# Optimization experiments

Measured on AMD Instinct MI355X. Metric: run time of the kernel, lower is better.

Reference implementation:

```python
import jax, jax.numpy as jnp
import numpy as np

HEADS = 8
EMBED = 128
HEAD_DIM = EMBED // HEADS


def setup_inputs() -> dict:
    key = jax.random.key(0)
    ks = jax.random.split(key, 6)
    s = 0.05
    return {
        "x": jax.random.normal(ks[0], (8, 128, 128, 128), dtype=jnp.float32),
        "Wq": jax.random.normal(ks[1], (HEAD_DIM, HEAD_DIM), dtype=jnp.float32) * s,
        "Wk": jax.random.normal(ks[2], (HEAD_DIM, HEAD_DIM), dtype=jnp.float32) * s,
        "Wv": jax.random.normal(ks[3], (HEAD_DIM, HEAD_DIM), dtype=jnp.float32) * s,
        "Wo": jax.random.normal(ks[4], (EMBED, EMBED), dtype=jnp.float32) * s,
        "bo": jnp.zeros((EMBED,), dtype=jnp.float32),
    }


def reference(x, Wq, Wk, Wv, Wo, bo):
    # is_width=False: attend along the H axis. x: [N, C, H, W]
    y = jnp.transpose(x, (0, 3, 2, 1))  # [N, W, H, C]
    N, D1, D2, C = y.shape
    y = y.reshape(N * D1, D2, HEADS, HEAD_DIM)  # [n, k, h, d]
    # nn.Linear applies y @ W.T
    q = jnp.einsum("nkhd,ed->nkhe", y, Wq)
    k = jnp.einsum("nkhd,ed->nkhe", y, Wk)
    v = jnp.einsum("nkhd,ed->nkhe", y, Wv)
    energy = jnp.einsum("nqhd,nkhd->nhqk", q, k)
    scale = jnp.asarray(EMBED, energy.dtype) ** 0.5  # note: original divides by sqrt(embed_size)
    attn = jax.nn.softmax(energy / scale, axis=-1)
    out = jnp.einsum("nhqk,nkhd->nqhd", attn, v).reshape(N, D1, D2, C)
    out = jnp.einsum("nqkc,ec->nqke", out, Wo) + bo
    return jnp.transpose(out, (0, 3, 2, 1))  # back to [N, C, H, W]
```

## Files before the change

kernel.cpp:

```cpp
#include <hip/hip_runtime.h>
#include <hip/hip_fp16.h>


typedef __attribute__((ext_vector_type(4))) float f32x4;
typedef __attribute__((ext_vector_type(4))) _Float16 f16x4;
typedef __attribute__((ext_vector_type(2))) __fp16 fp16x2r;
typedef __attribute__((ext_vector_type(8))) short bf16x8;

__device__ __forceinline__ unsigned int bf16_rne(float x) {
    unsigned int u = __float_as_uint(x);
    return (u + 0x7fffu + ((u >> 16) & 1u)) >> 16;
}
__device__ __forceinline__ unsigned int pack_half2(float a, float b) {
    __half2 h = __floats2half2_rn(a, b);
    return *reinterpret_cast<unsigned int*>(&h);
}

__global__ __launch_bounds__(1024, 4) void axattn_attn(
    const float* __restrict__ x,
    const float* __restrict__ Wq,
    const float* __restrict__ Wk,
    const float* __restrict__ Wv,
    const float* __restrict__ Wo,
    unsigned short* __restrict__ Wob,
    unsigned short* __restrict__ AO)
{
    int bb  = blockIdx.x;
    int xcd = bb & 7;
    int nh  = bb >> 3;
    int n0  = nh >> 3;
    int h   = nh & 7;
    int tid = threadIdx.x;
    int wvi = tid >> 6;
    int l   = tid & 63;
    int lr  = l & 15;
    int lg  = l >> 4;
    int w0  = xcd * 16;
    int w   = w0 + wvi;

    if (tid < 32) {
        int i = bb * 32 + tid;
        Wob[i] = (unsigned short)bf16_rne(Wo[i]);
    }

    __shared__ unsigned int xs[16 * 1280];

    {
        int q   = tid & 3;
        int row = (tid >> 2) & 127;
        int c2b = tid >> 9;
        const float* gp0 = x + ((size_t)(n0 * 128 + h * 16) * 128 + row) * 128 + w0 + q * 4;
        float4 va[4], vb[4];
        #pragma unroll
        for (int it = 0; it < 4; ++it) {
            const float* gp = gp0 + (size_t)(2 * (it * 2 + c2b)) * 16384;
            va[it] = *(const float4*)gp;
            vb[it] = *(const float4*)(gp + 16384);
        }
        #pragma unroll
        for (int it = 0; it < 4; ++it) {
            int c2 = it * 2 + c2b;
            unsigned int* dp = xs + (q * 4) * 1280 + row * 10 + c2;
            dp[0]    = pack_half2(va[it].x, vb[it].x);
            dp[1280] = pack_half2(va[it].y, vb[it].y);
            dp[2560] = pack_half2(va[it].z, vb[it].z);
            dp[3840] = pack_half2(va[it].w, vb[it].w);
        }
    }

    const float qsc = 0.088388347648318447f * 1.4426950408889634f;
    const f32x4 zf = {0.f, 0.f, 0.f, 0.f};

    float4 wqf = *(const float4*)(Wq + lr * 16 + lg * 4);
    float4 wkf = *(const float4*)(Wk + lr * 16 + lg * 4);
    float4 wvf = *(const float4*)(Wv + lr * 16 + lg * 4);
    f16x4 fq = {(_Float16)wqf.x, (_Float16)wqf.y, (_Float16)wqf.z, (_Float16)wqf.w};
    f16x4 fk = {(_Float16)wkf.x, (_Float16)wkf.y, (_Float16)wkf.z, (_Float16)wkf.w};
    f16x4 fv = {(_Float16)wvf.x, (_Float16)wvf.y, (_Float16)wvf.z, (_Float16)wvf.w};

    __syncthreads();

    const char* yb = (const char*)xs + wvi * 5120 + lr * 40 + lg * 8;
    f16x4 yf[8];
    #pragma unroll
    for (int rt = 0; rt < 8; ++rt)
        yf[rt] = *(const f16x4*)(yb + rt * 640);

    f16x4 qb[8], ka[8], vb[8];
    #pragma unroll
    for (int t = 0; t < 8; ++t) {
        f32x4 qt = __builtin_amdgcn_mfma_f32_16x16x16f16(fq, yf[t], zf, 0, 0, 0);
        f32x4 kt = __builtin_amdgcn_mfma_f32_16x16x16f16(fk, yf[t], zf, 0, 0, 0);
        f32x4 vt = __builtin_amdgcn_mfma_f32_16x16x16f16(yf[t], fv, zf, 0, 0, 0);
        qb[t] = (f16x4){(_Float16)(qt[0] * qsc), (_Float16)(qt[1] * qsc),
                        (_Float16)(qt[2] * qsc), (_Float16)(qt[3] * qsc)};
        ka[t] = (f16x4){(_Float16)kt[0], (_Float16)kt[1], (_Float16)kt[2], (_Float16)kt[3]};
        vb[t] = (f16x4){(_Float16)vt[0], (_Float16)vt[1], (_Float16)vt[2], (_Float16)vt[3]};
    }

    unsigned short* aob = AO + ((size_t)(n0 * 128 + w) * 128 + lg * 4) * 128 + h * 16 + lr;

    #pragma unroll
    for (int qt = 0; qt < 8; ++qt) {
        f32x4 s[8];
        #pragma unroll
        for (int kt = 0; kt < 8; ++kt)
            s[kt] = __builtin_amdgcn_mfma_f32_16x16x16f16(ka[kt], qb[qt], zf, 0, 0, 0);
        float sum = 0.f;
        f16x4 pa[8];
        #pragma unroll
        for (int kt = 0; kt < 8; ++kt) {
            float p0 = __builtin_amdgcn_exp2f(s[kt][0]);
            float p1 = __builtin_amdgcn_exp2f(s[kt][1]);
            float p2 = __builtin_amdgcn_exp2f(s[kt][2]);
            float p3 = __builtin_amdgcn_exp2f(s[kt][3]);
            sum += (p0 + p1) + (p2 + p3);
            union { fp16x2r h2[2]; f16x4 h4; } up;
            up.h2[0] = __builtin_amdgcn_cvt_pkrtz(p0, p1);
            up.h2[1] = __builtin_amdgcn_cvt_pkrtz(p2, p3);
            pa[kt] = up.h4;
        }
        sum += __shfl_xor(sum, 16);
        sum += __shfl_xor(sum, 32);
        f32x4 oA = zf, oB = zf;
        #pragma unroll
        for (int kt = 0; kt < 4; ++kt) {
            oA = __builtin_amdgcn_mfma_f32_16x16x16f16(pa[kt],     vb[kt],     oA, 0, 0, 0);
            oB = __builtin_amdgcn_mfma_f32_16x16x16f16(pa[kt + 4], vb[kt + 4], oB, 0, 0, 0);
        }
        f32x4 o = oA + oB;
        float rl = 1.f / sum;
        #pragma unroll
        for (int r = 0; r < 4; ++r) {
            float rs = __shfl(rl, lg * 4 + r);
            aob[((size_t)qt * 16 + r) * 128] = (unsigned short)bf16_rne(o[r] * rs);
        }
    }
}

__global__ __launch_bounds__(256) void axattn_proj(
    const unsigned short* __restrict__ AOb,
    const unsigned short* __restrict__ Wob,
    const float* __restrict__ bo,
    float* __restrict__ out)
{
    int bb  = blockIdx.x;
    int wh  = bb & 1;
    int s   = (bb >> 1) & 127;
    int n0  = bb >> 8;
    int tid = threadIdx.x;
    int wv  = tid >> 6;
    int l   = tid & 63;
    int lr  = l & 15;
    int lg  = l >> 4;
    int lk  = lg * 8;
    int eb  = wv * 32;

    __shared__ char as_[64 * 272];

    const unsigned short* wp_ = Wob + (size_t)(eb + lr) * 128 + lk;
    bf16x8 a0[4], a1[4];
    #pragma unroll
    for (int ct = 0; ct < 4; ++ct) {
        a0[ct] = *(const bf16x8*)(wp_ + ct * 32);
        a1[ct] = *(const bf16x8*)(wp_ + 16 * 128 + ct * 32);
    }

    {
        uint4 t4[4];
        #pragma unroll
        for (int it = 0; it < 4; ++it) {
            int flat = it * 256 + tid;
            int row  = flat >> 4;
            int seg  = flat & 15;
            t4[it] = *((const uint4*)(AOb
                + ((size_t)(n0 * 128 + wh * 64 + row) * 128 + s) * 128) + seg);
        }
        #pragma unroll
        for (int it = 0; it < 4; ++it) {
            int flat = it * 256 + tid;
            int row  = flat >> 4;
            int seg  = flat & 15;
            *(uint4*)(as_ + row * 272 + seg * 16) = t4[it];
        }
    }
    __syncthreads();

    f32x4 acc[2][4];
    #pragma unroll
    for (int mi = 0; mi < 2; ++mi)
        #pragma unroll
        for (int ni = 0; ni < 4; ++ni)
            acc[mi][ni] = (f32x4){0.f, 0.f, 0.f, 0.f};

    #pragma unroll
    for (int ct = 0; ct < 4; ++ct) {
        #pragma unroll
        for (int ni = 0; ni < 4; ++ni) {
            bf16x8 b = *(const bf16x8*)(as_ + (ni * 16 + lr) * 272 + (lk + ct * 32) * 2);
            acc[0][ni] = __builtin_amdgcn_mfma_f32_16x16x32_bf16(a0[ct], b, acc[0][ni], 0, 0, 0);
            acc[1][ni] = __builtin_amdgcn_mfma_f32_16x16x32_bf16(a1[ct], b, acc[1][ni], 0, 0, 0);
        }
    }

    int r4 = lg * 4;
    #pragma unroll
    for (int mi = 0; mi < 2; ++mi) {
        #pragma unroll
        for (int r = 0; r < 4; ++r) {
            int e = eb + mi * 16 + r4 + r;
            float bv = bo[e];
            float* orow = out + ((size_t)(n0 * 128 + e) * 128 + s) * 128 + wh * 64 + lr;
            #pragma unroll
            for (int ni = 0; ni < 4; ++ni)
                orow[ni * 16] = acc[mi][ni][r] + bv;
        }
    }
}

extern "C" void kernel_launch(void* const* d_in, const int* in_sizes, int n_in,
                              void* d_out, int out_size, void* d_ws, size_t ws_size,
                              hipStream_t stream) {
    const float* x  = (const float*)d_in[0];
    const float* Wq = (const float*)d_in[1];
    const float* Wk = (const float*)d_in[2];
    const float* Wv = (const float*)d_in[3];
    const float* Wo = (const float*)d_in[4];
    const float* bo = (const float*)d_in[5];
    float* out = (float*)d_out;

    unsigned short* AOb = (unsigned short*)d_ws;
    unsigned short* Wob = (unsigned short*)((char*)d_ws + (32u << 20));

    axattn_attn<<<512, 1024, 0, stream>>>(x, Wq, Wk, Wv, Wo, Wob, AOb);
    axattn_proj<<<2048, 256, 0, stream>>>(AOb, Wob, bo, out);
}
```

Before: 158.5 us.

## Process two heads per attention block with prefetched second-head loads

Each attention block now uses 512 threads covering 8 W columns and handles two heads in sequence instead of one head over 16 columns. The global loads for the second head are issued before the first head's compute, so their latency can overlap with it, and results are staged into a second LDS buffer. This costs more registers held across the compute phase and changes the block shape, which may lower occupancy.

New measurement: 168.0 us. 6.0% more time.

```diff
diff --git a/kernel.cpp b/kernel.cpp
--- a/kernel.cpp
+++ b/kernel.cpp
@@ -16,7 +16,70 @@
     return *reinterpret_cast<unsigned int*>(&h);
 }
 
-__global__ __launch_bounds__(1024, 4) void axattn_attn(
+__device__ __forceinline__ void attn_compute(
+    const unsigned int* xsbuf, int wvi, int lr, int lg,
+    f16x4 fq, f16x4 fk, f16x4 fv, float qsc,
+    unsigned short* __restrict__ aob)
+{
+    const f32x4 zf = {0.f, 0.f, 0.f, 0.f};
+
+    const char* yb = (const char*)xsbuf + wvi * 5120 + lr * 40 + lg * 8;
+    f16x4 yf[8];
+    #pragma unroll
+    for (int rt = 0; rt < 8; ++rt)
+        yf[rt] = *(const f16x4*)(yb + rt * 640);
+
+    f16x4 qb[8], ka[8], vb[8];
+    #pragma unroll
+    for (int t = 0; t < 8; ++t) {
+        f32x4 qt = __builtin_amdgcn_mfma_f32_16x16x16f16(fq, yf[t], zf, 0, 0, 0);
+        f32x4 kt = __builtin_amdgcn_mfma_f32_16x16x16f16(fk, yf[t], zf, 0, 0, 0);
+        f32x4 vt = __builtin_amdgcn_mfma_f32_16x16x16f16(yf[t], fv, zf, 0, 0, 0);
+        qb[t] = (f16x4){(_Float16)(qt[0] * qsc), (_Float16)(qt[1] * qsc),
+                        (_Float16)(qt[2] * qsc), (_Float16)(qt[3] * qsc)};
+        ka[t] = (f16x4){(_Float16)kt[0], (_Float16)kt[1], (_Float16)kt[2], (_Float16)kt[3]};
+        vb[t] = (f16x4){(_Float16)vt[0], (_Float16)vt[1], (_Float16)vt[2], (_Float16)vt[3]};
+    }
+
+    #pragma unroll
+    for (int qt = 0; qt < 8; ++qt) {
+        f32x4 s[8];
+        #pragma unroll
+        for (int kt = 0; kt < 8; ++kt)
+            s[kt] = __builtin_amdgcn_mfma_f32_16x16x16f16(ka[kt], qb[qt], zf, 0, 0, 0);
+        float sum = 0.f;
+        f16x4 pa[8];
+        #pragma unroll
+        for (int kt = 0; kt < 8; ++kt) {
+            float p0 = __builtin_amdgcn_exp2f(s[kt][0]);
+            float p1 = __builtin_amdgcn_exp2f(s[kt][1]);
+            float p2 = __builtin_amdgcn_exp2f(s[kt][2]);
+            float p3 = __builtin_amdgcn_exp2f(s[kt][3]);
+            sum += (p0 + p1) + (p2 + p3);
+            union { fp16x2r h2[2]; f16x4 h4; } up;
+            up.h2[0] = __builtin_amdgcn_cvt_pkrtz(p0, p1);
+            up.h2[1] = __builtin_amdgcn_cvt_pkrtz(p2, p3);
+            pa[kt] = up.h4;
+        }
+        sum += __shfl_xor(sum, 16);
+        sum += __shfl_xor(sum, 32);
+        f32x4 oA = zf, oB = zf;
+        #pragma unroll
+        for (int kt = 0; kt < 4; ++kt) {
+            oA = __builtin_amdgcn_mfma_f32_16x16x16f16(pa[kt],     vb[kt],     oA, 0, 0, 0);
+            oB = __builtin_amdgcn_mfma_f32_16x16x16f16(pa[kt + 4], vb[kt + 4], oB, 0, 0, 0);
+        }
+        f32x4 o = oA + oB;
+        float rl = 1.f / sum;
+        #pragma unroll
+        for (int r = 0; r < 4; ++r) {
+            float rs = __shfl(rl, lg * 4 + r);
+            aob[((size_t)qt * 16 + r) * 128] = (unsigned short)bf16_rne(o[r] * rs);
+        }
+    }
+}
+
+__global__ __launch_bounds__(512, 4) void axattn_attn(
     const float* __restrict__ x,
     const float* __restrict__ Wq,
     const float* __restrict__ Wk,
@@ -27,29 +90,34 @@
 {
     int bb  = blockIdx.x;
     int xcd = bb & 7;
-    int nh  = bb >> 3;
-    int n0  = nh >> 3;
-    int h   = nh & 7;
+    int k   = bb >> 3;
+    int wp  = k & 1;
+    int t2  = k >> 1;
+    int hp  = t2 & 3;
+    int n0  = t2 >> 2;
     int tid = threadIdx.x;
     int wvi = tid >> 6;
     int l   = tid & 63;
     int lr  = l & 15;
     int lg  = l >> 4;
-    int w0  = xcd * 16;
+    int w0  = xcd * 16 + wp * 8;
     int w   = w0 + wvi;
+    int h0  = hp * 2;
 
     if (tid < 32) {
         int i = bb * 32 + tid;
         Wob[i] = (unsigned short)bf16_rne(Wo[i]);
     }
 
-    __shared__ unsigned int xs[16 * 1280];
+    __shared__ unsigned int xs[2][8 * 1280];
+
+    int q   = tid & 1;
+    int row = (tid >> 1) & 127;
+    int c2b = tid >> 8;
+    const float* gpb = x + ((size_t)(n0 * 128) * 128 + row) * 128 + w0 + q * 4;
 
     {
-        int q   = tid & 3;
-        int row = (tid >> 2) & 127;
-        int c2b = tid >> 9;
-        const float* gp0 = x + ((size_t)(n0 * 128 + h * 16) * 128 + row) * 128 + w0 + q * 4;
+        const float* gp0 = gpb + (size_t)(h0 * 16) * 16384;
         float4 va[4], vb[4];
         #pragma unroll
         for (int it = 0; it < 4; ++it) {
@@ -60,7 +128,7 @@
         #pragma unroll
         for (int it = 0; it < 4; ++it) {
             int c2 = it * 2 + c2b;
-            unsigned int* dp = xs + (q * 4) * 1280 + row * 10 + c2;
+            unsigned int* dp = xs[0] + (q * 4) * 1280 + row * 10 + c2;
             dp[0]    = pack_half2(va[it].x, vb[it].x);
             dp[1280] = pack_half2(va[it].y, vb[it].y);
             dp[2560] = pack_half2(va[it].z, vb[it].z);
@@ -69,7 +137,6 @@
     }
 
     const float qsc = 0.088388347648318447f * 1.4426950408889634f;
-    const f32x4 zf = {0.f, 0.f, 0.f, 0.f};
 
     float4 wqf = *(const float4*)(Wq + lr * 16 + lg * 4);
     float4 wkf = *(const float4*)(Wk + lr * 16 + lg * 4);
@@ -80,62 +147,32 @@
 
     __syncthreads();
 
-    const char* yb = (const char*)xs + wvi * 5120 + lr * 40 + lg * 8;
-    f16x4 yf[8];
-    #pragma unroll
-    for (int rt = 0; rt < 8; ++rt)
-        yf[rt] = *(const f16x4*)(yb + rt * 640);
-
-    f16x4 qb[8], ka[8], vb[8];
-    #pragma unroll
-    for (int t = 0; t < 8; ++t) {
-        f32x4 qt = __builtin_amdgcn_mfma_f32_16x16x16f16(fq, yf[t], zf, 0, 0, 0);
-        f32x4 kt = __builtin_amdgcn_mfma_f32_16x16x16f16(fk, yf[t], zf, 0, 0, 0);
-        f32x4 vt = __builtin_amdgcn_mfma_f32_16x16x16f16(yf[t], fv, zf, 0, 0, 0);
-        qb[t] = (f16x4){(_Float16)(qt[0] * qsc), (_Float16)(qt[1] * qsc),
-                        (_Float16)(qt[2] * qsc), (_Float16)(qt[3] * qsc)};
-        ka[t] = (f16x4){(_Float16)kt[0], (_Float16)kt[1], (_Float16)kt[2], (_Float16)kt[3]};
-        vb[t] = (f16x4){(_Float16)vt[0], (_Float16)vt[1], (_Float16)vt[2], (_Float16)vt[3]};
-    }
-
-    unsigned short* aob = AO + ((size_t)(n0 * 128 + w) * 128 + lg * 4) * 128 + h * 16 + lr;
-
-    #pragma unroll
-    for (int qt = 0; qt < 8; ++qt) {
-        f32x4 s[8];
-        #pragma unroll
-        for (int kt = 0; kt < 8; ++kt)
-            s[kt] = __builtin_amdgcn_mfma_f32_16x16x16f16(ka[kt], qb[qt], zf, 0, 0, 0);
-        float sum = 0.f;
-        f16x4 pa[8];
-        #pragma unroll
-        for (int kt = 0; kt < 8; ++kt) {
-            float p0 = __builtin_amdgcn_exp2f(s[kt][0]);
-            float p1 = __builtin_amdgcn_exp2f(s[kt][1]);
-            float p2 = __builtin_amdgcn_exp2f(s[kt][2]);
-            float p3 = __builtin_amdgcn_exp2f(s[kt][3]);
-            sum += (p0 + p1) + (p2 + p3);
-            union { fp16x2r h2[2]; f16x4 h4; } up;
-            up.h2[0] = __builtin_amdgcn_cvt_pkrtz(p0, p1);
-            up.h2[1] = __builtin_amdgcn_cvt_pkrtz(p2, p3);
-            pa[kt] = up.h4;
-        }
-        sum += __shfl_xor(sum, 16);
-        sum += __shfl_xor(sum, 32);
-        f32x4 oA = zf, oB = zf;
-        #pragma unroll
-        for (int kt = 0; kt < 4; ++kt) {
-            oA = __builtin_amdgcn_mfma_f32_16x16x16f16(pa[kt],     vb[kt],     oA, 0, 0, 0);
-            oB = __builtin_amdgcn_mfma_f32_16x16x16f16(pa[kt + 4], vb[kt + 4], oB, 0, 0, 0);
-        }
-        f32x4 o = oA + oB;
-        float rl = 1.f / sum;
-        #pragma unroll
-        for (int r = 0; r < 4; ++r) {
-            float rs = __shfl(rl, lg * 4 + r);
-            aob[((size_t)qt * 16 + r) * 128] = (unsigned short)bf16_rne(o[r] * rs);
-        }
-    }
+    float4 va1[4], vb1[4];
+    {
+        const float* gp1 = gpb + (size_t)((h0 + 1) * 16) * 16384;
+        #pragma unroll
+        for (int it = 0; it < 4; ++it) {
+            const float* gp = gp1 + (size_t)(2 * (it * 2 + c2b)) * 16384;
+            va1[it] = *(const float4*)gp;
+            vb1[it] = *(const float4*)(gp + 16384);
+        }
+    }
+
+    unsigned short* aob0 = AO + ((size_t)(n0 * 128 + w) * 128 + lg * 4) * 128 + h0 * 16 + lr;
+    attn_compute(xs[0], wvi, lr, lg, fq, fk, fv, qsc, aob0);
+
+    #pragma unroll
+    for (int it = 0; it < 4; ++it) {
+        int c2 = it * 2 + c2b;
+        unsigned int* dp = xs[1] + (q * 4) * 1280 + row * 10 + c2;
+        dp[0]    = pack_half2(va1[it].x, vb1[it].x);
+        dp[1280] = pack_half2(va1[it].y, vb1[it].y);
+        dp[2560] = pack_half2(va1[it].z, vb1[it].z);
+        dp[3840] = pack_half2(va1[it].w, vb1[it].w);
+    }
+    __syncthreads();
+
+    attn_compute(xs[1], wvi, lr, lg, fq, fk, fv, qsc, aob0 + 16);
 }
 
 __global__ __launch_bounds__(256) void axattn_proj(
@@ -232,6 +269,6 @@
     unsigned short* AOb = (unsigned short*)d_ws;
     unsigned short* Wob = (unsigned short*)((char*)d_ws + (32u << 20));
 
-    axattn_attn<<<512, 1024, 0, stream>>>(x, Wq, Wk, Wv, Wo, Wob, AOb);
+    axattn_attn<<<512, 512, 0, stream>>>(x, Wq, Wk, Wv, Wo, Wob, AOb);
     axattn_proj<<<2048, 256, 0, stream>>>(AOb, Wob, bo, out);
 }
```
